# Performance work log

Hardware: AMD Instinct MI355X
Metric: run time of the kernel (lower is better)

The kernel has to match this reference:

```python
import jax, jax.numpy as jnp
import numpy as np

N_DOF = 7
HIDDEN = 256
BATCH = 32768
L_DIAG_OFFSET = 1e-3
FRICTION_EPS = 100.0


def setup_inputs() -> dict:
    key = jax.random.key(0)
    ks = jax.random.split(key, 16)
    n, H, B = N_DOF, HIDDEN, BATCH
    ntril = n * (n - 1) // 2

    def xavier(k, shape):
        fan_out, fan_in = shape
        std = (2.0 / (fan_in + fan_out)) ** 0.5
        return jax.random.normal(k, shape, jnp.float32) * std

    return {
        "q":   jax.random.normal(ks[0], (B, n), jnp.float32),
        "qd":  jax.random.normal(ks[1], (B, n), jnp.float32),
        "qdd": jax.random.normal(ks[2], (B, n), jnp.float32),
        # MLP trunk (hidden_depth = 3)
        "W0": xavier(ks[3], (H, n)),  "b0": jnp.zeros((H,), jnp.float32),
        "W1": xavier(ks[4], (H, H)),  "b1": jnp.zeros((H,), jnp.float32),
        "W2": xavier(ks[5], (H, H)),  "b2": jnp.zeros((H,), jnp.float32),
        # heads: gravity g, Cholesky diagonal, Cholesky strict-lower
        "Wg":  xavier(ks[6], (n, H)),     "bg":  jnp.zeros((n,), jnp.float32),
        "Wld": xavier(ks[7], (n, H)),     "bld": jnp.zeros((n,), jnp.float32),
        "Wlt": xavier(ks[8], (ntril, H)), "blt": jnp.zeros((ntril,), jnp.float32),
        # friction model parameters (init 0.1 each)
        "fd": jnp.full((n,), 0.1, jnp.float32),
        "fc": jnp.full((n,), 0.1, jnp.float32),
        "fs": jnp.full((n,), 0.1, jnp.float32),
        "fv": jnp.full((n,), 0.1, jnp.float32),
    }


def reference(q, qd, qdd, W0, b0, W1, b1, W2, b2, Wg, bg, Wld, bld, Wlt, blt,
              fd, fc, fs, fv):
    n = N_DOF
    B = q.shape[0]
    sp = jax.nn.softplus

    def net(qq):  # qq: [n] single sample
        h = sp(W0 @ qq + b0)
        h = sp(W1 @ h + b1)
        h = sp(W2 @ h + b2)
        g = Wg @ h + bg                      # [n]
        Ld_raw = Wld @ h + bld               # [n]
        Ld = sp(Ld_raw)                      # softplus diag activation
        Lt = Wlt @ h + blt                   # [n_tril]
        return (Ld, Lt), (g, Ld, Lt, Ld_raw)

    # per-sample Jacobians of (L_diag, L_tril) wrt q (forward mode, n_dof tangents)
    (jLd, jLt), (g, Ld, Lt, Ld_raw) = jax.vmap(jax.jacfwd(net, has_aux=True))(q)
    # jLd: [B,n,n], jLt: [B,ntril,n]

    idx = np.arange(n)
    rows, cols = np.tril_indices(n, -1)

    L = (jnp.zeros((B, n, n), q.dtype)
         .at[:, idx, idx].set(Ld)
         .at[:, rows, cols].set(Lt)
         + L_DIAG_OFFSET * jnp.eye(n, dtype=q.dtype))          # [B,n,n]
    L_dq = (jnp.zeros((B, n, n, n), q.dtype)
            .at[:, idx, idx, :].set(jLd)
            .at[:, rows, cols, :].set(jLt))                    # [B,n,n,n] (last = dq)

    LT = jnp.swapaxes(L, 1, 2)
    L_dqT = jnp.swapaxes(L_dq, 1, 2)

    Hm = jnp.einsum('bij,bjk->bik', L, LT)                      # mass matrix
    L_dt = jnp.einsum('bijc,bc->bij', L_dq, qd)                 # dL/dt
    L_dtT = jnp.swapaxes(L_dt, 1, 2)
    H_dt = jnp.einsum('bij,bjk->bik', L, L_dtT) + jnp.einsum('bij,bjk->bik', L_dt, LT)
    H_dq = (jnp.einsum('bijc,bjk->bikc', L_dq, LT)
            + jnp.einsum('bij,bjkc->bikc', L, L_dqT))           # [B,n,n,n]
    H_dq_qd = jnp.einsum('bijc,bj->bic', H_dq, qd)
    qdT_H_dq_qd = jnp.einsum('bi,bic->bc', qd, H_dq_qd)
    c = jnp.einsum('bij,bj->bi', H_dt, qd) - 0.5 * qdT_H_dq_qd  # Coriolis

    fv_c = jnp.clip(fv, 1e-3, None)
    tau_fric = (fc + fs * jnp.exp(-qd ** 2 / fv_c)) * jnp.tanh(FRICTION_EPS * qd) + fd * qd

    tau_pred = jnp.einsum('bij,bj->bi', Hm, qdd) + c + g + tau_fric
    return (tau_pred, Hm, c, g, tau_fric, Ld_raw)
```

## Files before the change

### kernel.cpp

```cpp
#include <hip/hip_runtime.h>
#include <cmath>

#define NDOF 7
#define HID  256
#define SPW  8
#define NCOL 64

typedef __bf16 bf16x8 __attribute__((ext_vector_type(8)));
typedef float  f32x4  __attribute__((ext_vector_type(4)));

#define OFF_W2 65536
#define OFF_WH 131072
#define OFF_W0 143360
#define WS_TOT 151552

__device__ __forceinline__ float softplus_fast(float x){
    float e = __expf(-fabsf(x));
    return fmaxf(x, 0.0f) + __logf(1.0f + e);
}
__device__ __forceinline__ float sigmoid_fast(float x){
    float e  = __expf(-fabsf(x));
    float rc = 1.0f / (1.0f + e);
    return (x >= 0.0f) ? rc : e * rc;
}
__device__ __forceinline__ float tanh_fast(float y){
    float e2 = __expf(-2.0f * fabsf(y));
    float t  = (1.0f - e2) / (1.0f + e2);
    return (y >= 0.0f) ? t : -t;
}

__global__ void convert_weights(const float* __restrict__ W1, const float* __restrict__ W2,
                                const float* __restrict__ Wg, const float* __restrict__ Wld,
                                const float* __restrict__ Wlt, const float* __restrict__ W0,
                                __bf16* __restrict__ ws)
{
    int i = blockIdx.x * 256 + threadIdx.x;
    if (i < OFF_W2)        ws[i] = (__bf16)W1[i];
    else if (i < OFF_WH)   ws[i] = (__bf16)W2[i - OFF_W2];
    else if (i < OFF_W0) {
        int j = i - OFF_WH;
        int r = j >> 8, k = j & 255;
        float v = 0.0f;
        if (r < 7)       v = Wg [r * HID + k];
        else if (r < 14) v = Wld[(r - 7) * HID + k];
        else if (r < 35) v = Wlt[(r - 14) * HID + k];
        ws[i] = (__bf16)v;
    } else if (i < WS_TOT) {
        int j = i - OFF_W0;
        int r = j >> 5, k = j & 31;
        ws[i] = (__bf16)((k < 7) ? W0[r * 7 + k] : 0.0f);
    }
}

template<int KK>
__device__ __forceinline__ void mlp_layer(
    const __bf16* __restrict__ Wb, int astride, const float* __restrict__ bp,
    __bf16* Xs, __bf16 (*sgbuf)[264],
    int w, int lo, int hi, const int* scol, bool prim)
{
    f32x4 acc[4][4];
    #pragma unroll
    for (int mi = 0; mi < 4; ++mi)
        #pragma unroll
        for (int ni = 0; ni < 4; ++ni) acc[mi][ni] = (f32x4){0.f,0.f,0.f,0.f};

    #pragma unroll 2
    for (int kk = 0; kk < KK; ++kk){
        const int k0 = kk * 32 + hi * 8;
        bf16x8 a[4], bfr[4];
        #pragma unroll
        for (int mi = 0; mi < 4; ++mi)
            a[mi] = *reinterpret_cast<const bf16x8*>(Wb + (w * 64 + mi * 16 + lo) * astride + k0);
        #pragma unroll
        for (int ni = 0; ni < 4; ++ni){
            int col = ni * 16 + lo;
            bfr[ni] = *reinterpret_cast<const bf16x8*>(Xs + col * HID + (k0 ^ ((col & 7) << 3)));
        }
        #pragma unroll
        for (int mi = 0; mi < 4; ++mi)
            #pragma unroll
            for (int ni = 0; ni < 4; ++ni)
                acc[mi][ni] = __builtin_amdgcn_mfma_f32_16x16x32_bf16(a[mi], bfr[ni], acc[mi][ni], 0, 0, 0);
    }
    __syncthreads();

    float h[4][4];
    #pragma unroll
    for (int mi = 0; mi < 4; ++mi){
        const int row0 = w * 64 + mi * 16 + hi * 4;
        float4 b4 = *reinterpret_cast<const float4*>(bp + row0);
        union { uint2 u2; __bf16 b[4]; } sp;
        #pragma unroll
        for (int r = 0; r < 4; ++r){
            float z  = acc[mi][0][r] + ((const float*)&b4)[r];
            float e  = __expf(-fabsf(z));
            float rc = 1.0f / (1.0f + e);
            h[mi][r] = fmaxf(z, 0.0f) + __logf(1.0f + e);
            sp.b[r]  = (__bf16)((z >= 0.0f) ? rc : e * rc);
        }
        if (lo < 8) *reinterpret_cast<uint2*>(&sgbuf[lo][row0]) = sp.u2;
    }
    asm volatile("s_waitcnt lgkmcnt(0)" ::: "memory");

    #pragma unroll
    for (int mi = 0; mi < 4; ++mi){
        const int row0 = w * 64 + mi * 16 + hi * 4;
        #pragma unroll
        for (int ni = 0; ni < 4; ++ni){
            union { uint2 u2; __bf16 b[4]; } sg;
            sg.u2 = *reinterpret_cast<const uint2*>(&sgbuf[scol[ni]][row0]);
            int col = ni * 16 + lo;
            union { uint2 u2; __bf16 b[4]; } pk;
            #pragma unroll
            for (int r = 0; r < 4; ++r){
                float v = (ni == 0 && prim) ? h[mi][r] : (float)sg.b[r] * acc[mi][ni][r];
                pk.b[r] = (__bf16)v;
            }
            *reinterpret_cast<uint2*>(Xs + col * HID + (row0 ^ ((col & 7) << 3))) = pk.u2;
        }
    }
    __syncthreads();
}

__launch_bounds__(256, 4)
__global__ void dln_main(
    const float* __restrict__ q,  const float* __restrict__ qd, const float* __restrict__ qdd,
    const float* __restrict__ b0, const float* __restrict__ b1, const float* __restrict__ b2,
    const float* __restrict__ bg, const float* __restrict__ bld, const float* __restrict__ blt,
    const float* __restrict__ fd, const float* __restrict__ fc,
    const float* __restrict__ fs, const float* __restrict__ fv,
    const __bf16* __restrict__ wsb,
    float* __restrict__ out, int Btot)
{
    __shared__ __align__(16) unsigned char LDSB[32768];
    __shared__ __bf16 sgbuf[SPW][264];
    __shared__ float  qs[SPW][NDOF], qds_[SPW][NDOF], qdds_[SPW][NDOF];

    __bf16* Xs = (__bf16*)LDSB;

    const int tid = threadIdx.x;
    const int w   = tid >> 6;
    const int l   = tid & 63;
    const int lo  = l & 15;
    const int hi  = l >> 4;
    const int s0g = blockIdx.x * SPW;
    const bool prim = (lo < 8);

    if (tid < SPW * NDOF){
        int s = tid / NDOF, d = tid % NDOF;
        qs[s][d]    = q  [(s0g + s) * NDOF + d];
        qds_[s][d]  = qd [(s0g + s) * NDOF + d];
        qdds_[s][d] = qdd[(s0g + s) * NDOF + d];
    }

    int scol[4];
    #pragma unroll
    for (int ni = 0; ni < 4; ++ni){
        int col  = ni * 16 + lo;
        scol[ni] = (col < 8) ? col : (col - 8) / 7;
    }

    {
        int col = tid >> 2, part = tid & 3;
        uint4 z4 = {0,0,0,0};
        *reinterpret_cast<uint4*>(Xs + col * HID + part * 16)     = z4;
        *reinterpret_cast<uint4*>(Xs + col * HID + part * 16 + 8) = z4;
    }
    __syncthreads();
    if (tid < 56){
        int s = tid / 7, d = tid % 7;
        Xs[s * HID + (d ^ ((s & 7) << 3))] = (__bf16)qs[s][d];
        int c = 8 + s * 7 + d;
        Xs[c * HID + (d ^ ((c & 7) << 3))] = (__bf16)1.0f;
    }
    __syncthreads();

    mlp_layer<1>(wsb + OFF_W0, 32,  b0, Xs, sgbuf, w, lo, hi, scol, prim);
    mlp_layer<8>(wsb,          HID, b1, Xs, sgbuf, w, lo, hi, scol, prim);
    mlp_layer<8>(wsb + OFF_W2, HID, b2, Xs, sgbuf, w, lo, hi, scol, prim);

    f32x4 hacc[4];
    #pragma unroll
    for (int ni = 0; ni < 4; ++ni) hacc[ni] = (f32x4){0.f,0.f,0.f,0.f};
    if (w < 3){
        const __bf16* Wh = wsb + OFF_WH;
        #pragma unroll 2
        for (int kk = 0; kk < 8; ++kk){
            const int k0 = kk * 32 + hi * 8;
            bf16x8 a = *reinterpret_cast<const bf16x8*>(Wh + (w * 16 + lo) * HID + k0);
            #pragma unroll
            for (int ni = 0; ni < 4; ++ni){
                int col = ni * 16 + lo;
                bf16x8 bfr = *reinterpret_cast<const bf16x8*>(Xs + col * HID + (k0 ^ ((col & 7) << 3)));
                hacc[ni] = __builtin_amdgcn_mfma_f32_16x16x32_bf16(a, bfr, hacc[ni], 0, 0, 0);
            }
        }
    }
    __syncthreads();

    float* SCR = (float*)LDSB;
    float* TB  = (float*)LDSB + 2304;
    #define LSA(s,i,j) TB[(s)*49+(i)*7+(j)]
    #define VSH(s,i,j) TB[392+(s)*49+(i)*7+(j)]
    #define LDT(s,i,j) TB[784+(s)*49+(i)*7+(j)]
    #define UB(s,k)    TB[1176+(s)*8+(k)]
    #define WB2(s,k)   TB[1240+(s)*8+(k)]
    #define SGL(s,k)   TB[1304+(s)*8+(k)]
    #define LDR(s,k)   TB[1368+(s)*8+(k)]

    if (w < 3){
        #pragma unroll
        for (int ni = 0; ni < 4; ++ni)
            #pragma unroll
            for (int r = 0; r < 4; ++r){
                int row = w * 16 + hi * 4 + r;
                if (row < 35) SCR[row * 64 + ni * 16 + lo] = hacc[ni][r];
            }
    }
    __syncthreads();

    {
        const int s = tid >> 5;
        const int t = tid & 31;

        if (t < 7){
            int i = t;
            float lr = SCR[(7 + i) * 64 + s] + bld[i];
            LDR(s, i) = lr;
            SGL(s, i) = sigmoid_fast(lr);
            for (int j = 0; j < 7; ++j){
                float val;
                if (j == i)      val = softplus_fast(lr) + 1e-3f;
                else if (j < i)  val = SCR[(14 + (i*(i-1))/2 + j) * 64 + s] + blt[(i*(i-1))/2 + j];
                else             val = 0.f;
                LSA(s, i, j) = val;
            }
        }
        __syncthreads();

        auto LDQ = [&](int i, int j, int c)->float{
            if (i == j) return SGL(s, i) * SCR[(7 + i) * 64 + 8 + s * 7 + c];
            if (i >  j) return SCR[(14 + (i*(i-1))/2 + j) * 64 + 8 + s * 7 + c];
            return 0.f;
        };

        if (t < 7){
            float u = 0.f;
            for (int j = 0; j < 7; ++j) u = fmaf(qds_[s][j], LSA(s, j, t), u);
            UB(s, t) = u;
            for (int m = 0; m < 7; ++m){
                float v = 0.f;
                for (int j = 0; j < 7; ++j) v = fmaf(qds_[s][j], LDQ(j, m, t), v);
                VSH(s, m, t) = v;
            }
            for (int k = 0; k < 7; ++k){
                float a = 0.f;
                for (int c2 = 0; c2 < 7; ++c2) a = fmaf(LDQ(t, k, c2), qds_[s][c2], a);
                LDT(s, t, k) = a;
            }
        }
        __syncthreads();

        if (t < 7){
            float w2 = 0.f;
            for (int c2 = 0; c2 < 7; ++c2) w2 = fmaf(VSH(s, t, c2), qds_[s][c2], w2);
            WB2(s, t) = w2;
        }
        __syncthreads();

        if (t < 7){
            const int i  = t;
            const int Sg = s0g + s;
            float c1 = 0.f;
            for (int k = 0; k < 7; ++k)
                c1 += LSA(s, i, k) * WB2(s, k) + LDT(s, i, k) * UB(s, k);
            float qh = 0.f;
            for (int m = 0; m < 7; ++m) qh = fmaf(UB(s, m), VSH(s, m, i), qh);
            float cfin = c1 - qh;
            float hm[7];
            for (int j = 0; j < 7; ++j){
                float a = 0.f;
                for (int k = 0; k < 7; ++k) a = fmaf(LSA(s, i, k), LSA(s, j, k), a);
                hm[j] = a;
            }
            float gv  = SCR[i * 64 + s] + bg[i];
            float qdv = qds_[s][i];
            float fvc = fmaxf(fv[i], 1e-3f);
            float tf  = (fc[i] + fs[i] * __expf(-qdv * qdv / fvc)) * tanh_fast(100.0f * qdv) + fd[i] * qdv;
            float tp  = cfin + gv + tf;
            for (int j = 0; j < 7; ++j) tp = fmaf(hm[j], qdds_[s][j], tp);

            const int B = Btot;
            out[Sg * 7 + i] = tp;
            float* o1 = out + (size_t)B * 7;
            for (int j = 0; j < 7; ++j) o1[(size_t)Sg * 49 + i * 7 + j] = hm[j];
            out[(size_t)B * 56 + Sg * 7 + i] = cfin;
            out[(size_t)B * 63 + Sg * 7 + i] = gv;
            out[(size_t)B * 70 + Sg * 7 + i] = tf;
            out[(size_t)B * 77 + Sg * 7 + i] = LDR(s, i);
        }
    }
}

extern "C" void kernel_launch(void* const* d_in, const int* in_sizes, int n_in,
                              void* d_out, int out_size, void* d_ws, size_t ws_size,
                              hipStream_t stream) {
    const float* q   = (const float*)d_in[0];
    const float* qd  = (const float*)d_in[1];
    const float* qdd = (const float*)d_in[2];
    const float* W0  = (const float*)d_in[3];
    const float* b0  = (const float*)d_in[4];
    const float* W1  = (const float*)d_in[5];
    const float* b1  = (const float*)d_in[6];
    const float* W2  = (const float*)d_in[7];
    const float* b2  = (const float*)d_in[8];
    const float* Wg  = (const float*)d_in[9];
    const float* bg  = (const float*)d_in[10];
    const float* Wld = (const float*)d_in[11];
    const float* bld = (const float*)d_in[12];
    const float* Wlt = (const float*)d_in[13];
    const float* blt = (const float*)d_in[14];
    const float* fd  = (const float*)d_in[15];
    const float* fc  = (const float*)d_in[16];
    const float* fs  = (const float*)d_in[17];
    const float* fv  = (const float*)d_in[18];

    const int Btot = in_sizes[0] / NDOF;
    __bf16* wsb = (__bf16*)d_ws;

    convert_weights<<<dim3(WS_TOT / 256), dim3(256), 0, stream>>>(W1, W2, Wg, Wld, Wlt, W0, wsb);
    dln_main<<<dim3(Btot / SPW), dim3(256), 0, stream>>>(q, qd, qdd, b0, b1, b2,
                                                         bg, bld, blt,
                                                         fd, fc, fs, fv,
                                                         wsb, (float*)d_out, Btot);
}
```

Measured before the change: 267.4 us.

## Shuffle sigmoid gates, parallelize Lagrangian tail across 49 lanes, raise occupancy

The MLP layers now broadcast the sigmoid gate through wave shuffles instead of an LDS buffer with a wait. The per-sample mass-matrix and Coriolis tail moves from 7 threads per sample with several block barriers to one wave per sample using 49 lanes, shuffle reductions and a transposed scratch layout. Launch bounds rise to 5 waves per SIMD, the MFMA loops unroll further, and qd/qdd are read directly from global memory. The higher occupancy target and the deeper unrolling may force register spills.

```diff
diff --git a/kernel.cpp b/kernel.cpp
--- a/kernel.cpp
+++ b/kernel.cpp
@@ -55,8 +55,7 @@
 template<int KK>
 __device__ __forceinline__ void mlp_layer(
     const __bf16* __restrict__ Wb, int astride, const float* __restrict__ bp,
-    __bf16* Xs, __bf16 (*sgbuf)[264],
-    int w, int lo, int hi, const int* scol, bool prim)
+    __bf16* Xs, int w, int lo, int hi, const int* srcl, bool prim)
 {
     f32x4 acc[4][4];
     #pragma unroll
@@ -64,7 +63,7 @@
         #pragma unroll
         for (int ni = 0; ni < 4; ++ni) acc[mi][ni] = (f32x4){0.f,0.f,0.f,0.f};
 
-    #pragma unroll 2
+    #pragma unroll 4
     for (int kk = 0; kk < KK; ++kk){
         const int k0 = kk * 32 + hi * 8;
         bf16x8 a[4], bfr[4];
@@ -84,36 +83,27 @@
     }
     __syncthreads();
 
-    float h[4][4];
     #pragma unroll
     for (int mi = 0; mi < 4; ++mi){
         const int row0 = w * 64 + mi * 16 + hi * 4;
         float4 b4 = *reinterpret_cast<const float4*>(bp + row0);
-        union { uint2 u2; __bf16 b[4]; } sp;
+        float h[4], sg[4];
         #pragma unroll
         for (int r = 0; r < 4; ++r){
             float z  = acc[mi][0][r] + ((const float*)&b4)[r];
             float e  = __expf(-fabsf(z));
             float rc = 1.0f / (1.0f + e);
-            h[mi][r] = fmaxf(z, 0.0f) + __logf(1.0f + e);
-            sp.b[r]  = (__bf16)((z >= 0.0f) ? rc : e * rc);
-        }
-        if (lo < 8) *reinterpret_cast<uint2*>(&sgbuf[lo][row0]) = sp.u2;
-    }
-    asm volatile("s_waitcnt lgkmcnt(0)" ::: "memory");
-
-    #pragma unroll
-    for (int mi = 0; mi < 4; ++mi){
-        const int row0 = w * 64 + mi * 16 + hi * 4;
+            h[r]  = fmaxf(z, 0.0f) + __logf(1.0f + e);
+            sg[r] = (z >= 0.0f) ? rc : e * rc;
+        }
         #pragma unroll
         for (int ni = 0; ni < 4; ++ni){
-            union { uint2 u2; __bf16 b[4]; } sg;
-            sg.u2 = *reinterpret_cast<const uint2*>(&sgbuf[scol[ni]][row0]);
             int col = ni * 16 + lo;
             union { uint2 u2; __bf16 b[4]; } pk;
             #pragma unroll
             for (int r = 0; r < 4; ++r){
-                float v = (ni == 0 && prim) ? h[mi][r] : (float)sg.b[r] * acc[mi][ni][r];
+                float sgb = __shfl(sg[r], srcl[ni]);
+                float v   = (ni == 0 && prim) ? h[r] : sgb * acc[mi][ni][r];
                 pk.b[r] = (__bf16)v;
             }
             *reinterpret_cast<uint2*>(Xs + col * HID + (row0 ^ ((col & 7) << 3))) = pk.u2;
@@ -122,7 +112,7 @@
     __syncthreads();
 }
 
-__launch_bounds__(256, 4)
+__launch_bounds__(256, 5)
 __global__ void dln_main(
     const float* __restrict__ q,  const float* __restrict__ qd, const float* __restrict__ qdd,
     const float* __restrict__ b0, const float* __restrict__ b1, const float* __restrict__ b2,
@@ -133,9 +123,6 @@
     float* __restrict__ out, int Btot)
 {
     __shared__ __align__(16) unsigned char LDSB[32768];
-    __shared__ __bf16 sgbuf[SPW][264];
-    __shared__ float  qs[SPW][NDOF], qds_[SPW][NDOF], qdds_[SPW][NDOF];
-
     __bf16* Xs = (__bf16*)LDSB;
 
     const int tid = threadIdx.x;
@@ -146,18 +133,12 @@
     const int s0g = blockIdx.x * SPW;
     const bool prim = (lo < 8);
 
-    if (tid < SPW * NDOF){
-        int s = tid / NDOF, d = tid % NDOF;
-        qs[s][d]    = q  [(s0g + s) * NDOF + d];
-        qds_[s][d]  = qd [(s0g + s) * NDOF + d];
-        qdds_[s][d] = qdd[(s0g + s) * NDOF + d];
-    }
-
-    int scol[4];
+    int srcl[4];
     #pragma unroll
     for (int ni = 0; ni < 4; ++ni){
         int col  = ni * 16 + lo;
-        scol[ni] = (col < 8) ? col : (col - 8) / 7;
+        int s    = (col < 8) ? col : (col - 8) / 7;
+        srcl[ni] = (l & ~15) | s;
     }
 
     {
@@ -168,23 +149,23 @@
     }
     __syncthreads();
     if (tid < 56){
-        int s = tid / 7, d = tid % 7;
-        Xs[s * HID + (d ^ ((s & 7) << 3))] = (__bf16)qs[s][d];
+        int s = tid / 7, d = tid - s * 7;
+        Xs[s * HID + (d ^ ((s & 7) << 3))] = (__bf16)q[(s0g + s) * NDOF + d];
         int c = 8 + s * 7 + d;
         Xs[c * HID + (d ^ ((c & 7) << 3))] = (__bf16)1.0f;
     }
     __syncthreads();
 
-    mlp_layer<1>(wsb + OFF_W0, 32,  b0, Xs, sgbuf, w, lo, hi, scol, prim);
-    mlp_layer<8>(wsb,          HID, b1, Xs, sgbuf, w, lo, hi, scol, prim);
-    mlp_layer<8>(wsb + OFF_W2, HID, b2, Xs, sgbuf, w, lo, hi, scol, prim);
+    mlp_layer<1>(wsb + OFF_W0, 32,  b0, Xs, w, lo, hi, srcl, prim);
+    mlp_layer<8>(wsb,          HID, b1, Xs, w, lo, hi, srcl, prim);
+    mlp_layer<8>(wsb + OFF_W2, HID, b2, Xs, w, lo, hi, srcl, prim);
 
     f32x4 hacc[4];
     #pragma unroll
     for (int ni = 0; ni < 4; ++ni) hacc[ni] = (f32x4){0.f,0.f,0.f,0.f};
     if (w < 3){
         const __bf16* Wh = wsb + OFF_WH;
-        #pragma unroll 2
+        #pragma unroll 4
         for (int kk = 0; kk < 8; ++kk){
             const int k0 = kk * 32 + hi * 8;
             bf16x8 a = *reinterpret_cast<const bf16x8*>(Wh + (w * 16 + lo) * HID + k0);
@@ -198,15 +179,10 @@
     }
     __syncthreads();
 
-    float* SCR = (float*)LDSB;
-    float* TB  = (float*)LDSB + 2304;
-    #define LSA(s,i,j) TB[(s)*49+(i)*7+(j)]
-    #define VSH(s,i,j) TB[392+(s)*49+(i)*7+(j)]
-    #define LDT(s,i,j) TB[784+(s)*49+(i)*7+(j)]
-    #define UB(s,k)    TB[1176+(s)*8+(k)]
-    #define WB2(s,k)   TB[1240+(s)*8+(k)]
-    #define SGL(s,k)   TB[1304+(s)*8+(k)]
-    #define LDR(s,k)   TB[1368+(s)*8+(k)]
+    float* SCRT = (float*)LDSB;
+    float* SGb  = (float*)(LDSB + 10496);
+    float* UV   = (float*)(LDSB + 10752);
+    float* LL   = (float*)(LDSB + 11264);
 
     if (w < 3){
         #pragma unroll
@@ -214,90 +190,130 @@
             #pragma unroll
             for (int r = 0; r < 4; ++r){
                 int row = w * 16 + hi * 4 + r;
-                if (row < 35) SCR[row * 64 + ni * 16 + lo] = hacc[ni][r];
+                if (row < 35) SCRT[(ni * 16 + lo) * 41 + row] = hacc[ni][r];
             }
     }
     __syncthreads();
 
-    {
-        const int s = tid >> 5;
-        const int t = tid & 31;
-
-        if (t < 7){
-            int i = t;
-            float lr = SCR[(7 + i) * 64 + s] + bld[i];
-            LDR(s, i) = lr;
-            SGL(s, i) = sigmoid_fast(lr);
-            for (int j = 0; j < 7; ++j){
-                float val;
-                if (j == i)      val = softplus_fast(lr) + 1e-3f;
-                else if (j < i)  val = SCR[(14 + (i*(i-1))/2 + j) * 64 + s] + blt[(i*(i-1))/2 + j];
-                else             val = 0.f;
-                LSA(s, i, j) = val;
+    const bool t49 = (l < 49);
+    const int  tt  = t49 ? l : 0;
+    const int  r   = tt / 7;
+    const int  c   = tt - r * 7;
+    const int  B   = Btot;
+    float* oH = out + (size_t)B * 7;
+    float* oC = out + (size_t)B * 56;
+    float* oG = out + (size_t)B * 63;
+    float* oF = out + (size_t)B * 70;
+    float* oL = out + (size_t)B * 77;
+
+    for (int p = 0; p < 2; ++p){
+        const int ss = p * 4 + w;
+        const int Sg = __builtin_amdgcn_readfirstlane(s0g + ss);
+        float qdv[7], qddv[7];
+        #pragma unroll
+        for (int d = 0; d < 7; ++d){ qdv[d] = qd[Sg * 7 + d]; qddv[d] = qdd[Sg * 7 + d]; }
+
+        const int colP  = ss * 41;
+        const int tri_r = (r * (r - 1)) >> 1;
+
+        float ldraw = SCRT[colP + 7 + r] + bld[r];
+        float sg_r  = sigmoid_fast(ldraw);
+        float Lrr   = softplus_fast(ldraw) + 1e-3f;
+        float Lij   = 0.f;
+        if (c < r)       Lij = SCRT[colP + 14 + tri_r + c] + blt[tri_r + c];
+        else if (c == r) Lij = Lrr;
+
+        if (t49)           LL[ss * 52 + tt]   = Lij;
+        if (t49 && r == c) SGb[ss * 8 + r]    = sg_r;
+
+        float ux = qdv[r] * Lij;
+        { float xs;
+          xs = __shfl(ux, l + 7);  ux += (r + 1 <= 6) ? xs : 0.f;
+          xs = __shfl(ux, l + 14); ux += (r + 2 <= 6) ? xs : 0.f;
+          xs = __shfl(ux, l + 28); ux += (r + 4 <= 6) ? xs : 0.f; }
+        if (t49 && r == 0) UV[ss * 16 + c] = ux;
+
+        asm volatile("s_waitcnt lgkmcnt(0)" ::: "memory");
+        __builtin_amdgcn_sched_barrier(0);
+
+        float sgv[7];
+        #pragma unroll
+        for (int jj = 0; jj < 7; ++jj) sgv[jj] = SGb[ss * 8 + jj];
+
+        const int colT = (8 + ss * 7 + c) * 41;
+        float v = 0.f;
+        #pragma unroll
+        for (int jj = 0; jj < 7; ++jj){
+            constexpr int triT[7] = {0,0,1,3,6,10,15};
+            int   row = (jj == r) ? (7 + jj) : (14 + triT[jj] + r);
+            float x   = SCRT[colT + row];
+            float val = (jj == r) ? sgv[jj] * x : ((jj > r) ? x : 0.f);
+            v = fmaf(qdv[jj], val, v);
+        }
+
+        {
+            int   rowF   = (r == c) ? (7 + r) : (14 + tri_r + c);
+            float scaleF = (r == c) ? sg_r : ((r > c) ? 1.f : 0.f);
+            float acc2 = 0.f;
+            #pragma unroll
+            for (int cc = 0; cc < 7; ++cc)
+                acc2 = fmaf(qdv[cc], SCRT[(8 + ss * 7 + cc) * 41 + rowF], acc2);
+            v = v;
+            float ldt = acc2 * scaleF;
+
+            float wx = v * qdv[c];
+            { float xs;
+              xs = __shfl(wx, l + 1); wx += (c + 1 <= 6) ? xs : 0.f;
+              xs = __shfl(wx, l + 2); wx += (c + 2 <= 6) ? xs : 0.f;
+              xs = __shfl(wx, l + 4); wx += (c + 4 <= 6) ? xs : 0.f; }
+            if (t49 && c == 0) UV[ss * 16 + 8 + r] = wx;
+
+            asm volatile("s_waitcnt lgkmcnt(0)" ::: "memory");
+            __builtin_amdgcn_sched_barrier(0);
+
+            float u_c  = UV[ss * 16 + c];
+            float u_r  = UV[ss * 16 + r];
+            float w2_c = UV[ss * 16 + 8 + c];
+
+            float qx = u_r * v;
+            { float xs;
+              xs = __shfl(qx, l + 7);  qx += (r + 1 <= 6) ? xs : 0.f;
+              xs = __shfl(qx, l + 14); qx += (r + 2 <= 6) ? xs : 0.f;
+              xs = __shfl(qx, l + 28); qx += (r + 4 <= 6) ? xs : 0.f; }
+
+            float cx = Lij * w2_c + ldt * u_c;
+            { float xs;
+              xs = __shfl(cx, l + 1); cx += (c + 1 <= 6) ? xs : 0.f;
+              xs = __shfl(cx, l + 2); cx += (c + 2 <= 6) ? xs : 0.f;
+              xs = __shfl(cx, l + 4); cx += (c + 4 <= 6) ? xs : 0.f; }
+
+            float hm = 0.f;
+            #pragma unroll
+            for (int k = 0; k < 7; ++k)
+                hm = fmaf(LL[ss * 52 + r * 7 + k], LL[ss * 52 + c * 7 + k], hm);
+
+            float tx = hm * qddv[c];
+            { float xs;
+              xs = __shfl(tx, l + 1); tx += (c + 1 <= 6) ? xs : 0.f;
+              xs = __shfl(tx, l + 2); tx += (c + 2 <= 6) ? xs : 0.f;
+              xs = __shfl(tx, l + 4); tx += (c + 4 <= 6) ? xs : 0.f; }
+
+            float qh_r = __shfl(qx, r);
+            float gv   = SCRT[colP + r] + bg[r];
+            float qdr  = qdv[r];
+            float fvc  = fmaxf(fv[r], 1e-3f);
+            float tf   = (fc[r] + fs[r] * __expf(-qdr * qdr / fvc)) * tanh_fast(100.0f * qdr) + fd[r] * qdr;
+            float cfin = cx - qh_r;
+            float tau  = cfin + gv + tf + tx;
+
+            if (t49) oH[(size_t)Sg * 49 + tt] = hm;
+            if (t49 && c == 0){
+                out[Sg * 7 + r] = tau;
+                oC[Sg * 7 + r]  = cfin;
+                oG[Sg * 7 + r]  = gv;
+                oF[Sg * 7 + r]  = tf;
+                oL[Sg * 7 + r]  = ldraw;
             }
-        }
-        __syncthreads();
-
-        auto LDQ = [&](int i, int j, int c)->float{
-            if (i == j) return SGL(s, i) * SCR[(7 + i) * 64 + 8 + s * 7 + c];
-            if (i >  j) return SCR[(14 + (i*(i-1))/2 + j) * 64 + 8 + s * 7 + c];
-            return 0.f;
-        };
-
-        if (t < 7){
-            float u = 0.f;
-            for (int j = 0; j < 7; ++j) u = fmaf(qds_[s][j], LSA(s, j, t), u);
-            UB(s, t) = u;
-            for (int m = 0; m < 7; ++m){
-                float v = 0.f;
-                for (int j = 0; j < 7; ++j) v = fmaf(qds_[s][j], LDQ(j, m, t), v);
-                VSH(s, m, t) = v;
-            }
-            for (int k = 0; k < 7; ++k){
-                float a = 0.f;
-                for (int c2 = 0; c2 < 7; ++c2) a = fmaf(LDQ(t, k, c2), qds_[s][c2], a);
-                LDT(s, t, k) = a;
-            }
-        }
-        __syncthreads();
-
-        if (t < 7){
-            float w2 = 0.f;
-            for (int c2 = 0; c2 < 7; ++c2) w2 = fmaf(VSH(s, t, c2), qds_[s][c2], w2);
-            WB2(s, t) = w2;
-        }
-        __syncthreads();
-
-        if (t < 7){
-            const int i  = t;
-            const int Sg = s0g + s;
-            float c1 = 0.f;
-            for (int k = 0; k < 7; ++k)
-                c1 += LSA(s, i, k) * WB2(s, k) + LDT(s, i, k) * UB(s, k);
-            float qh = 0.f;
-            for (int m = 0; m < 7; ++m) qh = fmaf(UB(s, m), VSH(s, m, i), qh);
-            float cfin = c1 - qh;
-            float hm[7];
-            for (int j = 0; j < 7; ++j){
-                float a = 0.f;
-                for (int k = 0; k < 7; ++k) a = fmaf(LSA(s, i, k), LSA(s, j, k), a);
-                hm[j] = a;
-            }
-            float gv  = SCR[i * 64 + s] + bg[i];
-            float qdv = qds_[s][i];
-            float fvc = fmaxf(fv[i], 1e-3f);
-            float tf  = (fc[i] + fs[i] * __expf(-qdv * qdv / fvc)) * tanh_fast(100.0f * qdv) + fd[i] * qdv;
-            float tp  = cfin + gv + tf;
-            for (int j = 0; j < 7; ++j) tp = fmaf(hm[j], qdds_[s][j], tp);
-
-            const int B = Btot;
-            out[Sg * 7 + i] = tp;
-            float* o1 = out + (size_t)B * 7;
-            for (int j = 0; j < 7; ++j) o1[(size_t)Sg * 49 + i * 7 + j] = hm[j];
-            out[(size_t)B * 56 + Sg * 7 + i] = cfin;
-            out[(size_t)B * 63 + Sg * 7 + i] = gv;
-            out[(size_t)B * 70 + Sg * 7 + i] = tf;
-            out[(size_t)B * 77 + Sg * 7 + i] = LDR(s, i);
         }
     }
 }
```

New measurement: 488.8 us. +82.8%, slower.
